# Optimization experiments

Measured on AMD Instinct MI355X. Metric: run time of the kernel, lower is better.

Reference implementation:

```python
import jax, jax.numpy as jnp
import numpy as np


def _attention(v, W, static_hidden, dec_hidden):
    # static_hidden: [B,N,H], dec_hidden: [B,1,H], v: [1,1,H], W: [1,H,2H]
    hidden = jnp.concatenate(
        [static_hidden, jnp.broadcast_to(dec_hidden, static_hidden.shape)], axis=2
    )  # [B,N,2H]
    e = jnp.tanh(jnp.einsum('bnk,hk->bnh', hidden, W[0]))  # W @ hidden^T, done row-wise
    scores = jnp.einsum('bnh,h->bn', e, v[0, 0])  # [B,N]
    return jax.nn.softmax(scores, axis=1)[:, None, :]  # [B,1,N]


def _gru_step(x, h, w_ih, w_hh, b_ih, b_hh):
    # x: [B,H] input, h: [B,H] prev hidden; PyTorch gate order: r | z | n
    gx = x @ w_ih.T + b_ih  # [B,3H]
    gh = h @ w_hh.T + b_hh  # [B,3H]
    H = h.shape[-1]
    r = jax.nn.sigmoid(gx[:, :H] + gh[:, :H])
    z = jax.nn.sigmoid(gx[:, H:2 * H] + gh[:, H:2 * H])
    n = jnp.tanh(gx[:, 2 * H:] + r * gh[:, 2 * H:])
    return (1.0 - z) * n + z * h


def _pointer_scores(v, W, static_hidden, context, state_embedding):
    # energy = cat(static, context, state_emb) -> [B,N,3H]
    energy = jnp.concatenate(
        [static_hidden,
         jnp.broadcast_to(context, static_hidden.shape),
         jnp.broadcast_to(state_embedding, static_hidden.shape)], axis=2)
    e = jnp.tanh(jnp.einsum('bnk,hk->bnh', energy, W[0]))  # [B,N,H]
    return jnp.einsum('bnh,h->bn', e, v[0, 0])  # [B,N]


def setup_inputs() -> dict:
    key = jax.random.key(0)
    B, N, H = 128, 512, 512
    ks = jax.random.split(key, 16)
    s = 0.05
    return {
        'static_hidden': jax.random.normal(ks[0], (B, N, H), jnp.float32),
        'state_embedding': jax.random.normal(ks[1], (B, 1, H), jnp.float32),
        'decoder_hidden': jax.random.normal(ks[2], (B, 1, H), jnp.float32),
        'target_hidden': jax.random.normal(ks[3], (B, 1, H), jnp.float32),
        'last_hh': jax.random.normal(ks[4], (1, B, H), jnp.float32),
        # Pointer params (note: target branch of the original reuses self.v/self.W)
        'ptr_v': jax.random.normal(ks[5], (1, 1, H), jnp.float32) * s,
        'ptr_W': jax.random.normal(ks[6], (1, H, 3 * H), jnp.float32) * s,
        # encoder attention params
        'enc_v': jax.random.normal(ks[7], (1, 1, H), jnp.float32) * s,
        'enc_W': jax.random.normal(ks[8], (1, H, 2 * H), jnp.float32) * s,
        # target attention params
        'tgt_v': jax.random.normal(ks[9], (1, 1, H), jnp.float32) * s,
        'tgt_W': jax.random.normal(ks[10], (1, H, 2 * H), jnp.float32) * s,
        # GRU (single layer) params
        'gru_w_ih': jax.random.normal(ks[11], (3 * H, H), jnp.float32) * s,
        'gru_w_hh': jax.random.normal(ks[12], (3 * H, H), jnp.float32) * s,
        'gru_b_ih': jax.random.normal(ks[13], (3 * H,), jnp.float32) * s,
        'gru_b_hh': jax.random.normal(ks[14], (3 * H,), jnp.float32) * s,
    }


def reference(static_hidden, state_embedding, decoder_hidden, target_hidden, last_hh,
              ptr_v, ptr_W, enc_v, enc_W, tgt_v, tgt_W,
              gru_w_ih, gru_w_hh, gru_b_ih, gru_b_hh):
    # GRU over seq len 1 (batch_first); dropout layers are identity (eval mode)
    h_new = _gru_step(decoder_hidden[:, 0, :], last_hh[0], gru_w_ih, gru_w_hh, gru_b_ih, gru_b_hh)
    rnn_out = h_new[:, None, :]          # [B,1,H]
    new_last_hh = h_new[None]            # [1,B,H]

    # encoder attention + context
    enc_attn = _attention(enc_v, enc_W, static_hidden, rnn_out)   # [B,1,N]
    context = jnp.matmul(enc_attn, static_hidden)                 # [B,1,H]
    probs = _pointer_scores(ptr_v, ptr_W, static_hidden, context, state_embedding)

    # target attention + context (original reuses self.v/self.W for scoring)
    tgt_attn = _attention(tgt_v, tgt_W, static_hidden, target_hidden)
    context_t = jnp.matmul(tgt_attn, static_hidden)
    probs_target = _pointer_scores(ptr_v, ptr_W, static_hidden, context_t, state_embedding)

    probs = 5.0 * probs + probs_target
    return (probs, new_last_hh)
```

## Files before the change

### kernel.cpp

```cpp
#include <hip/hip_runtime.h>
#include <math.h>

#define B 128
#define N 512
#define H 512

typedef __attribute__((ext_vector_type(8))) short short8;
typedef __attribute__((ext_vector_type(4))) float floatx4;

typedef const __attribute__((address_space(1))) unsigned int* gas_t;
typedef __attribute__((address_space(3))) unsigned int* las_t;

__device__ __forceinline__ void gl16(const void* g, void* l){
    __builtin_amdgcn_global_load_lds((gas_t)g, (las_t)l, 16, 0, 0);
}

__device__ __forceinline__ float sigmoidf_(float x){ return 1.0f/(1.0f+__expf(-x)); }

__device__ __forceinline__ float fast_tanh(float x){
    float t = __expf(-2.0f*fabsf(x));
    float r = __fdividef(1.0f - t, 1.0f + t);
    return copysignf(r, x);
}

__device__ __forceinline__ unsigned f2bf1(float f){
    unsigned u = __float_as_uint(f);
    u += 0x7FFFu + ((u>>16)&1u);
    return u>>16;
}
__device__ __forceinline__ unsigned pk2(float a, float b){
    return f2bf1(a) | (f2bf1(b)<<16);
}

__global__ __launch_bounds__(256) void k_cast_small(
    const float* __restrict__ encW, const float* __restrict__ tgtW,
    const float* __restrict__ ptrW, const float* __restrict__ wih,
    const float* __restrict__ whh,
    const float* __restrict__ dec, const float* __restrict__ lhh,
    const float* __restrict__ tgt, const float* __restrict__ sem,
    unsigned short* __restrict__ We_s, unsigned short* __restrict__ Wt_s,
    unsigned short* __restrict__ Wp_s, unsigned short* __restrict__ We_d,
    unsigned short* __restrict__ Wt_d, unsigned short* __restrict__ Wp_c,
    unsigned short* __restrict__ Wp_e, unsigned short* __restrict__ Wih_b,
    unsigned short* __restrict__ Whh_b,
    unsigned short* __restrict__ Xbf, unsigned short* __restrict__ Hbf,
    unsigned short* __restrict__ Tbf, unsigned short* __restrict__ Sbf)
{
    int r = blockIdx.x, t = threadIdx.x;
    if (r < 6656){
        const float* src; unsigned short* dst; int pitch, off, row;
        if (r < 512)      { src=encW; dst=We_s; pitch=2*H; off=0;   row=r; }
        else if (r<1024)  { src=tgtW; dst=Wt_s; pitch=2*H; off=0;   row=r-512; }
        else if (r<1536)  { src=ptrW; dst=Wp_s; pitch=3*H; off=0;   row=r-1024; }
        else if (r<2048)  { src=encW; dst=We_d; pitch=2*H; off=H;   row=r-1536; }
        else if (r<2560)  { src=tgtW; dst=Wt_d; pitch=2*H; off=H;   row=r-2048; }
        else if (r<3072)  { src=ptrW; dst=Wp_c; pitch=3*H; off=H;   row=r-2560; }
        else if (r<3584)  { src=ptrW; dst=Wp_e; pitch=3*H; off=2*H; row=r-3072; }
        else if (r<5120)  { src=wih;  dst=Wih_b;pitch=H;   off=0;   row=r-3584; }
        else              { src=whh;  dst=Whh_b;pitch=H;   off=0;   row=r-5120; }
        float2 v = *(const float2*)&src[(size_t)row*pitch + off + 2*t];
        *(unsigned*)&dst[(size_t)row*H + 2*t] = pk2(v.x, v.y);
    } else {
        int blk = r - 6656; int mat = blk >> 5;
        const float* src = mat==0?dec : mat==1?lhh : mat==2?tgt : sem;
        unsigned short* dst = mat==0?Xbf : mat==1?Hbf : mat==2?Tbf : Sbf;
        size_t i = ((size_t)(blk&31)*256 + t)*8;
        float4 lo = *(const float4*)&src[i];
        float4 hi = *(const float4*)&src[i+4];
        uint4 p;
        p.x = pk2(lo.x,lo.y); p.y = pk2(lo.z,lo.w);
        p.z = pk2(hi.x,hi.y); p.w = pk2(hi.z,hi.w);
        *(uint4*)&dst[i] = p;
    }
}

__device__ __forceinline__ void gemm128_tile(
    const unsigned short* __restrict__ Ab,
    const unsigned short* __restrict__ Bb,
    float* __restrict__ C, int ldc)
{
    __shared__ __align__(16) unsigned short As[128*64];
    __shared__ __align__(16) unsigned short Bs[128*64];
    int t = threadIdx.x;
    int lane = t & 63, wave = t >> 6;
    int wy = wave >> 1, wx = wave & 1;
    int li = lane & 15, quad = lane >> 4;

    floatx4 acc[4][4];
    #pragma unroll
    for (int i=0;i<4;++i)
      #pragma unroll
      for (int j=0;j<4;++j) acc[i][j] = (floatx4)(0.0f);

    for (int kt=0; kt<8; ++kt){
        int k0 = kt*64;
        #pragma unroll
        for (int c=0;c<4;++c){
            int s = c*256 + t;
            int row = s >> 3;
            int kb = (s & 7) ^ (row & 7);
            gl16(&Ab[(size_t)row*512 + k0 + kb*8], &As[(size_t)s*8]);
            gl16(&Bb[(size_t)row*512 + k0 + kb*8], &Bs[(size_t)s*8]);
        }
        __syncthreads();
        #pragma unroll
        for (int ks=0;ks<2;++ks){
            short8 af[4], bg[4];
            #pragma unroll
            for (int i=0;i<4;++i){
                int m = wy*64 + i*16 + li;
                int kb = (ks*4 + quad) ^ (m&7);
                af[i] = *(const short8*)&As[m*64 + kb*8];
            }
            #pragma unroll
            for (int j=0;j<4;++j){
                int h = wx*64 + j*16 + li;
                int kb = (ks*4 + quad) ^ (h&7);
                bg[j] = *(const short8*)&Bs[h*64 + kb*8];
            }
            #pragma unroll
            for (int i=0;i<4;++i)
              #pragma unroll
              for (int j=0;j<4;++j)
                acc[i][j] = __builtin_amdgcn_mfma_f32_16x16x32_bf16(af[i], bg[j], acc[i][j], 0,0,0);
        }
        __syncthreads();
    }
    #pragma unroll
    for (int i=0;i<4;++i)
      #pragma unroll
      for (int j=0;j<4;++j)
        #pragma unroll
        for (int rg=0;rg<4;++rg){
            int m = wy*64 + i*16 + quad*4 + rg;
            int n = wx*64 + j*16 + li;
            C[(size_t)m*ldc + n] = acc[i][j][rg];
        }
}

__device__ __forceinline__ void gemm128_tile_f32A(
    const float* __restrict__ Af,
    const unsigned short* __restrict__ Bb,
    float* __restrict__ C, int ldc)
{
    __shared__ __align__(16) unsigned short As[128*64];
    __shared__ __align__(16) unsigned short Bs[128*64];
    int t = threadIdx.x;
    int lane = t & 63, wave = t >> 6;
    int wy = wave >> 1, wx = wave & 1;
    int li = lane & 15, quad = lane >> 4;

    floatx4 acc[4][4];
    #pragma unroll
    for (int i=0;i<4;++i)
      #pragma unroll
      for (int j=0;j<4;++j) acc[i][j] = (floatx4)(0.0f);

    for (int kt=0; kt<8; ++kt){
        int k0 = kt*64;
        #pragma unroll
        for (int c=0;c<4;++c){
            int s = c*256 + t;
            int row = s >> 3;
            int kb = (s & 7) ^ (row & 7);
            gl16(&Bb[(size_t)row*512 + k0 + kb*8], &Bs[(size_t)s*8]);
            const float* src = Af + (size_t)row*512 + k0 + kb*8;
            float4 lo = *(const float4*)src;
            float4 hi = *(const float4*)(src+4);
            uint4 p;
            p.x = pk2(lo.x,lo.y); p.y = pk2(lo.z,lo.w);
            p.z = pk2(hi.x,hi.y); p.w = pk2(hi.z,hi.w);
            *(uint4*)&As[(size_t)s*8] = p;
        }
        __syncthreads();
        #pragma unroll
        for (int ks=0;ks<2;++ks){
            short8 af[4], bg[4];
            #pragma unroll
            for (int i=0;i<4;++i){
                int m = wy*64 + i*16 + li;
                int kb = (ks*4 + quad) ^ (m&7);
                af[i] = *(const short8*)&As[m*64 + kb*8];
            }
            #pragma unroll
            for (int j=0;j<4;++j){
                int h = wx*64 + j*16 + li;
                int kb = (ks*4 + quad) ^ (h&7);
                bg[j] = *(const short8*)&Bs[h*64 + kb*8];
            }
            #pragma unroll
            for (int i=0;i<4;++i)
              #pragma unroll
              for (int j=0;j<4;++j)
                acc[i][j] = __builtin_amdgcn_mfma_f32_16x16x32_bf16(af[i], bg[j], acc[i][j], 0,0,0);
        }
        __syncthreads();
    }
    #pragma unroll
    for (int i=0;i<4;++i)
      #pragma unroll
      for (int j=0;j<4;++j)
        #pragma unroll
        for (int rg=0;rg<4;++rg){
            int m = wy*64 + i*16 + quad*4 + rg;
            int n = wx*64 + j*16 + li;
            C[(size_t)m*ldc + n] = acc[i][j][rg];
        }
}

__global__ __launch_bounds__(256,2) void k_mega(
    const unsigned short* __restrict__ Xbf, const unsigned short* __restrict__ Hbf,
    const unsigned short* __restrict__ Wih_b, const unsigned short* __restrict__ Whh_b,
    float* __restrict__ gx, float* __restrict__ gh,
    const unsigned short* __restrict__ Tbf, const unsigned short* __restrict__ Sbf,
    const unsigned short* __restrict__ Wt_d, const unsigned short* __restrict__ Wp_e,
    float* __restrict__ d_tgt, float* __restrict__ d_se,
    const float* __restrict__ A, unsigned short* __restrict__ Abf)
{
    int blk = blockIdx.x;
    if (blk < 32){
        const unsigned short *Ab, *Bb; float* C; int ldc;
        if (blk < 24){
            int mat = blk / 12, nt = blk % 12;
            Ab = mat ? Hbf : Xbf;
            Bb = (mat ? Whh_b : Wih_b) + (size_t)nt*128*512;
            C = (mat ? gh : gx) + nt*128;
            ldc = 3*H;
        } else {
            int sub = blk - 24; int mat = sub >> 2, nt = sub & 3;
            Ab = mat==0 ? Tbf : Sbf;
            Bb = (mat==0 ? Wt_d : Wp_e) + (size_t)nt*128*512;
            C = (mat==0 ? d_tgt : d_se) + nt*128;
            ldc = H;
        }
        gemm128_tile(Ab, Bb, C, ldc);
    } else {
        int t = threadIdx.x;
        size_t i = ((size_t)(blk-32)*256 + t)*8;
        float4 lo = *(const float4*)&A[i];
        float4 hi = *(const float4*)&A[i+4];
        uint4 p;
        p.x = pk2(lo.x,lo.y); p.y = pk2(lo.z,lo.w);
        p.z = pk2(hi.x,hi.y); p.w = pk2(hi.z,hi.w);
        *(uint4*)&Abf[i] = p;
    }
}

__global__ __launch_bounds__(256) void k_gru_gate(const float* __restrict__ gx,
    const float* __restrict__ gh, const float* __restrict__ lhh,
    const float* __restrict__ bih, const float* __restrict__ bhh,
    float* __restrict__ out_hh, unsigned short* __restrict__ hnew_bf)
{
    int idx = blockIdx.x*256 + threadIdx.x;
    int b = idx >> 9, k = idx & 511;
    const float* gxb = gx + (size_t)b*(3*H);
    const float* ghb = gh + (size_t)b*(3*H);
    float r = sigmoidf_(gxb[k]     + bih[k]     + ghb[k]     + bhh[k]);
    float z = sigmoidf_(gxb[H+k]   + bih[H+k]   + ghb[H+k]   + bhh[H+k]);
    float n = tanhf(gxb[2*H+k] + bih[2*H+k] + r*(ghb[2*H+k] + bhh[2*H+k]));
    float h = (1.f-z)*n + z*lhh[idx];
    out_hh[idx] = h;
    hnew_bf[idx] = (unsigned short)f2bf1(h);
}

__global__ __launch_bounds__(256,2) void k_bias_enc(
    const unsigned short* __restrict__ HNbf, const unsigned short* __restrict__ We_d,
    float* __restrict__ d_enc)
{
    int nt = blockIdx.x;
    gemm128_tile(HNbf, We_d + (size_t)nt*128*512, d_enc + nt*128, H);
}

__global__ __launch_bounds__(256,2) void k_dptr_gemm(
    const float* __restrict__ ctx, const float* __restrict__ ctxt,
    const unsigned short* __restrict__ Wp_c,
    float* __restrict__ d_pe, float* __restrict__ d_pt)
{
    int blk = blockIdx.x;
    int mat = blk >> 2, nt = blk & 3;
    const float* Af = mat ? ctxt : ctx;
    const unsigned short* Bb = Wp_c + (size_t)nt*128*512;
    float* C = (mat ? d_pt : d_pe) + nt*128;
    gemm128_tile_f32A(Af, Bb, C, H);
}

template<bool BF16A>
__global__ __launch_bounds__(256,2) void k_scores_fused(
    const float* __restrict__ Af, const unsigned short* __restrict__ Abf,
    const unsigned short* __restrict__ We, const unsigned short* __restrict__ Wt,
    const float* __restrict__ d_enc, const float* __restrict__ d_tgt,
    const float* __restrict__ enc_v, const float* __restrict__ tgt_v,
    float* __restrict__ sc_e, float* __restrict__ sc_t)
{
    __shared__ __align__(16) unsigned short As[128*64];
    __shared__ __align__(16) unsigned short Be[128*64];
    __shared__ __align__(16) unsigned short Bt[128*64];
    __shared__ float red_e[2][128], red_t[2][128];
    int blk = blockIdx.x;
    int b = blk >> 2; int nt = blk & 3;
    int n0 = nt*128;
    int t = threadIdx.x;
    int lane = t & 63, wave = t >> 6;
    int wy = wave >> 1, wx = wave & 1;
    int li = lane & 15, quad = lane >> 4;

    float nse[4][4], nst[4][4];
    #pragma unroll
    for (int i=0;i<4;++i)
      #pragma unroll
      for (int rg=0;rg<4;++rg){ nse[i][rg]=0.f; nst[i][rg]=0.f; }

    for (int ht=0; ht<4; ++ht){
        int hb = ht*128;
        floatx4 acc_e[4][4], acc_t[4][4];
        #pragma unroll
        for (int i=0;i<4;++i)
          #pragma unroll
          for (int j=0;j<4;++j){ acc_e[i][j]=(floatx4)(0.0f); acc_t[i][j]=(floatx4)(0.0f); }

        for (int kt=0; kt<8; ++kt){
            int k0 = kt*64;
            #pragma unroll
            for (int c=0;c<4;++c){
                int s = c*256 + t;
                int row = s >> 3;
                int kb = (s & 7) ^ (row & 7);
                if constexpr (BF16A){
                    gl16(&Abf[(size_t)(b*N+n0+row)*H + k0 + kb*8], &As[(size_t)s*8]);
                } else {
                    const float* src = Af + (size_t)(b*N+n0+row)*H + k0 + kb*8;
                    float4 lo = *(const float4*)src;
                    float4 hi = *(const float4*)(src+4);
                    uint4 p;
                    p.x = pk2(lo.x,lo.y); p.y = pk2(lo.z,lo.w);
                    p.z = pk2(hi.x,hi.y); p.w = pk2(hi.z,hi.w);
                    *(uint4*)&As[(size_t)s*8] = p;
                }
                gl16(&We[(size_t)(hb+row)*H + k0 + kb*8], &Be[(size_t)s*8]);
                gl16(&Wt[(size_t)(hb+row)*H + k0 + kb*8], &Bt[(size_t)s*8]);
            }
            __syncthreads();
            #pragma unroll
            for (int ks=0;ks<2;++ks){
                short8 af[4], be[4], bt[4];
                #pragma unroll
                for (int i=0;i<4;++i){
                    int m = wy*64 + i*16 + li;
                    int kb = (ks*4 + quad) ^ (m&7);
                    af[i] = *(const short8*)&As[m*64 + kb*8];
                }
                #pragma unroll
                for (int j=0;j<4;++j){
                    int h = wx*64 + j*16 + li;
                    int kb = (ks*4 + quad) ^ (h&7);
                    be[j] = *(const short8*)&Be[h*64 + kb*8];
                    bt[j] = *(const short8*)&Bt[h*64 + kb*8];
                }
                #pragma unroll
                for (int i=0;i<4;++i)
                  #pragma unroll
                  for (int j=0;j<4;++j){
                    acc_e[i][j] = __builtin_amdgcn_mfma_f32_16x16x32_bf16(af[i], be[j], acc_e[i][j], 0,0,0);
                    acc_t[i][j] = __builtin_amdgcn_mfma_f32_16x16x32_bf16(af[i], bt[j], acc_t[i][j], 0,0,0);
                  }
            }
            __syncthreads();
        }
        #pragma unroll
        for (int j=0;j<4;++j){
            int hm = hb + wx*64 + j*16 + li;
            float dje = d_enc[b*H+hm], vje = enc_v[hm];
            float djt = d_tgt[b*H+hm], vjt = tgt_v[hm];
            #pragma unroll
            for (int i=0;i<4;++i)
              #pragma unroll
              for (int rg=0;rg<4;++rg){
                nse[i][rg] += vje * fast_tanh(acc_e[i][j][rg] + dje);
                nst[i][rg] += vjt * fast_tanh(acc_t[i][j][rg] + djt);
              }
        }
    }
    #pragma unroll
    for (int off=1; off<16; off<<=1)
      #pragma unroll
      for (int i=0;i<4;++i)
        #pragma unroll
        for (int rg=0;rg<4;++rg){
          nse[i][rg] += __shfl_xor(nse[i][rg], off);
          nst[i][rg] += __shfl_xor(nst[i][rg], off);
        }
    if (li==0){
        #pragma unroll
        for (int i=0;i<4;++i)
          #pragma unroll
          for (int rg=0;rg<4;++rg){
            red_e[wx][wy*64 + i*16 + quad*4 + rg] = nse[i][rg];
            red_t[wx][wy*64 + i*16 + quad*4 + rg] = nst[i][rg];
          }
    }
    __syncthreads();
    if (t < 128){
        sc_e[b*N + n0 + t] = red_e[0][t] + red_e[1][t];
    } else {
        int r2 = t - 128;
        sc_t[b*N + n0 + r2] = red_t[0][r2] + red_t[1][r2];
    }
}

template<bool BF16A>
__global__ __launch_bounds__(256) void k_smax_ctx(
    const float* __restrict__ Af, const unsigned short* __restrict__ Abf,
    const float* __restrict__ sc_e, const float* __restrict__ sc_t,
    float* __restrict__ ctx, float* __restrict__ ctxt)
{
    __shared__ float we[512], wt[512];
    __shared__ float buf[256];
    __shared__ float red[4][64][4];
    int b = blockIdx.x >> 2, q = blockIdx.x & 3;
    int t = threadIdx.x;

    {
        float x0 = sc_e[b*N+t], x1 = sc_e[b*N+t+256];
        float m = fmaxf(x0,x1);
        buf[t]=m; __syncthreads();
        for (int s2=128;s2>0;s2>>=1){ if(t<s2) buf[t]=fmaxf(buf[t],buf[t+s2]); __syncthreads(); }
        m = buf[0]; __syncthreads();
        float e0 = __expf(x0-m), e1 = __expf(x1-m);
        buf[t]=e0+e1; __syncthreads();
        for (int s2=128;s2>0;s2>>=1){ if(t<s2) buf[t]+=buf[t+s2]; __syncthreads(); }
        float inv = 1.0f/buf[0]; __syncthreads();
        we[t]=e0*inv; we[t+256]=e1*inv;
    }
    {
        float x0 = sc_t[b*N+t], x1 = sc_t[b*N+t+256];
        float m = fmaxf(x0,x1);
        buf[t]=m; __syncthreads();
        for (int s2=128;s2>0;s2>>=1){ if(t<s2) buf[t]=fmaxf(buf[t],buf[t+s2]); __syncthreads(); }
        m = buf[0]; __syncthreads();
        float e0 = __expf(x0-m), e1 = __expf(x1-m);
        buf[t]=e0+e1; __syncthreads();
        for (int s2=128;s2>0;s2>>=1){ if(t<s2) buf[t]+=buf[t+s2]; __syncthreads(); }
        float inv = 1.0f/buf[0]; __syncthreads();
        wt[t]=e0*inv; wt[t+256]=e1*inv;
    }
    __syncthreads();

    int p = t & 63, nq = t >> 6;
    int cp = q*64 + p;
    float ae0=0.f, ae1=0.f, at0=0.f, at1=0.f;
    if constexpr (BF16A){
        const unsigned* base = (const unsigned*)Abf + (size_t)(b*N + nq*128)*(H/2) + cp;
        for (int n=0;n<128;++n){
            unsigned u = base[(size_t)n*(H/2)];
            float lo = __uint_as_float(u<<16);
            float hi = __uint_as_float(u & 0xFFFF0000u);
            float e = we[nq*128+n], g = wt[nq*128+n];
            ae0 += e*lo; ae1 += e*hi; at0 += g*lo; at1 += g*hi;
        }
    } else {
        const float* base = Af + (size_t)(b*N + nq*128)*H + 2*cp;
        for (int n=0;n<128;++n){
            float2 v = *(const float2*)&base[(size_t)n*H];
            float e = we[nq*128+n], g = wt[nq*128+n];
            ae0 += e*v.x; ae1 += e*v.y; at0 += g*v.x; at1 += g*v.y;
        }
    }
    red[nq][p][0]=ae0; red[nq][p][1]=ae1; red[nq][p][2]=at0; red[nq][p][3]=at1;
    __syncthreads();
    if (t < 64){
        float s0=0.f,s1=0.f,s2=0.f,s3=0.f;
        #pragma unroll
        for (int k2=0;k2<4;++k2){
            s0+=red[k2][t][0]; s1+=red[k2][t][1]; s2+=red[k2][t][2]; s3+=red[k2][t][3];
        }
        int c2 = q*64 + t;
        ctx [(size_t)b*H + 2*c2]   = s0;
        ctx [(size_t)b*H + 2*c2+1] = s1;
        ctxt[(size_t)b*H + 2*c2]   = s2;
        ctxt[(size_t)b*H + 2*c2+1] = s3;
    }
}

template<bool BF16A>
__global__ __launch_bounds__(256,2) void k_probs_mfma(
    const float* __restrict__ Af, const unsigned short* __restrict__ Abf,
    const unsigned short* __restrict__ Wp,
    const float* __restrict__ d_pe, const float* __restrict__ d_pt,
    const float* __restrict__ d_se,
    const float* __restrict__ ptr_v, float* __restrict__ probs)
{
    __shared__ __align__(16) unsigned short As[128*64];
    __shared__ __align__(16) unsigned short Bs[128*64];
    __shared__ float red[2][128];
    int blk = blockIdx.x;
    int b = blk >> 2; int nt = blk & 3;
    int n0 = nt*128;

    int t = threadIdx.x;
    int lane = t & 63, wave = t >> 6;
    int wy = wave >> 1, wx = wave & 1;
    int li = lane & 15, quad = lane >> 4;

    float nsum[4][4];
    #pragma unroll
    for (int i=0;i<4;++i){ nsum[i][0]=0.f;nsum[i][1]=0.f;nsum[i][2]=0.f;nsum[i][3]=0.f; }

    for (int ht=0; ht<4; ++ht){
        int hb = ht*128;
        floatx4 acc[4][4];
        #pragma unroll
        for (int i=0;i<4;++i)
          #pragma unroll
          for (int j=0;j<4;++j) acc[i][j] = (floatx4)(0.0f);

        for (int kt=0; kt<8; ++kt){
            int k0 = kt*64;
            #pragma unroll
            for (int c=0;c<4;++c){
                int s = c*256 + t;
                int row = s >> 3;
                int kb = (s & 7) ^ (row & 7);
                if constexpr (BF16A){
                    gl16(&Abf[(size_t)(b*N+n0+row)*H + k0 + kb*8], &As[(size_t)s*8]);
                } else {
                    const float* src = Af + (size_t)(b*N+n0+row)*H + k0 + kb*8;
                    float4 lo = *(const float4*)src;
                    float4 hi = *(const float4*)(src+4);
                    uint4 p;
                    p.x = pk2(lo.x,lo.y); p.y = pk2(lo.z,lo.w);
                    p.z = pk2(hi.x,hi.y); p.w = pk2(hi.z,hi.w);
                    *(uint4*)&As[(size_t)s*8] = p;
                }
                gl16(&Wp[(size_t)(hb+row)*H + k0 + kb*8], &Bs[(size_t)s*8]);
            }
            __syncthreads();
            #pragma unroll
            for (int ks=0;ks<2;++ks){
                short8 af[4], bg[4];
                #pragma unroll
                for (int i=0;i<4;++i){
                    int m = wy*64 + i*16 + li;
                    int kb = (ks*4 + quad) ^ (m&7);
                    af[i] = *(const short8*)&As[m*64 + kb*8];
                }
                #pragma unroll
                for (int j=0;j<4;++j){
                    int h = wx*64 + j*16 + li;
                    int kb = (ks*4 + quad) ^ (h&7);
                    bg[j] = *(const short8*)&Bs[h*64 + kb*8];
                }
                #pragma unroll
                for (int i=0;i<4;++i)
                  #pragma unroll
                  for (int j=0;j<4;++j)
                    acc[i][j] = __builtin_amdgcn_mfma_f32_16x16x32_bf16(af[i], bg[j], acc[i][j], 0,0,0);
            }
            __syncthreads();
        }
        #pragma unroll
        for (int j=0;j<4;++j){
            int hm = hb + wx*64 + j*16 + li;
            float se = d_se[b*H + hm];
            float de = d_pe[b*H + hm] + se;
            float dt = d_pt[b*H + hm] + se;
            float vj = ptr_v[hm];
            #pragma unroll
            for (int i=0;i<4;++i)
              #pragma unroll
              for (int rg=0;rg<4;++rg){
                float s = acc[i][j][rg];
                nsum[i][rg] += vj * (5.0f*fast_tanh(s + de) + fast_tanh(s + dt));
              }
        }
    }
    #pragma unroll
    for (int off=1; off<16; off<<=1)
      #pragma unroll
      for (int i=0;i<4;++i)
        #pragma unroll
        for (int rg=0;rg<4;++rg)
          nsum[i][rg] += __shfl_xor(nsum[i][rg], off);
    if (li==0){
        #pragma unroll
        for (int i=0;i<4;++i)
          #pragma unroll
          for (int rg=0;rg<4;++rg)
            red[wx][wy*64 + i*16 + quad*4 + rg] = nsum[i][rg];
    }
    __syncthreads();
    if (t < 128)
        probs[b*N + n0 + t] = red[0][t] + red[1][t];
}

extern "C" void kernel_launch(void* const* d_in, const int* in_sizes, int n_in,
                              void* d_out, int out_size, void* d_ws, size_t ws_size,
                              hipStream_t stream)
{
    (void)in_sizes; (void)n_in; (void)out_size;
    const float* A    = (const float*)d_in[0];
    const float* sem  = (const float*)d_in[1];
    const float* dec  = (const float*)d_in[2];
    const float* tgt  = (const float*)d_in[3];
    const float* lhh  = (const float*)d_in[4];
    const float* ptrv = (const float*)d_in[5];
    const float* ptrW = (const float*)d_in[6];
    const float* encv = (const float*)d_in[7];
    const float* encW = (const float*)d_in[8];
    const float* tgtv = (const float*)d_in[9];
    const float* tgtW = (const float*)d_in[10];
    const float* wih  = (const float*)d_in[11];
    const float* whh  = (const float*)d_in[12];
    const float* bih  = (const float*)d_in[13];
    const float* bhh  = (const float*)d_in[14];

    float* probs_out = (float*)d_out;
    float* hh_out    = (float*)d_out + B*N;

    float* ws = (float*)d_ws;
    const size_t S = (size_t)B*H;
    float* d_enc = ws;
    float* d_tgt = ws + S;
    float* d_se  = ws + 2*S;
    float* sc_e  = ws + 3*S;
    float* sc_t  = ws + 4*S;
    float* ctx   = ws + 5*S;
    float* ctxt  = ws + 6*S;
    float* d_pe  = ws + 9*S;
    float* d_pt  = ws + 10*S;
    float* gx    = ws + 11*S;
    float* gh    = ws + 14*S;
    unsigned short* bfb  = (unsigned short*)(ws + 17*S);
    const size_t WH = (size_t)H*H;
    const size_t WG = (size_t)3*H*H;
    unsigned short* We_s  = bfb;
    unsigned short* Wt_s  = We_s + WH;
    unsigned short* Wp_s  = Wt_s + WH;
    unsigned short* We_d  = Wp_s + WH;
    unsigned short* Wt_d  = We_d + WH;
    unsigned short* Wp_c  = Wt_d + WH;
    unsigned short* Wp_e  = Wp_c + WH;
    unsigned short* Wih_b = Wp_e + WH;
    unsigned short* Whh_b = Wih_b + WG;
    unsigned short* Xbf   = Whh_b + WG;
    unsigned short* Hbf   = Xbf + S;
    unsigned short* Tbf   = Hbf + S;
    unsigned short* Sbf   = Tbf + S;
    unsigned short* HNbf  = Sbf + S;
    unsigned short* Abf   = HNbf + S;

    const size_t need_full = 17*S*sizeof(float)
        + (7*WH + 2*WG + 5*S + (size_t)B*N*H) * sizeof(unsigned short);
    const bool big = ws_size >= need_full;

    k_cast_small<<<6784, 256, 0, stream>>>(encW, tgtW, ptrW, wih, whh,
        dec, lhh, tgt, sem,
        We_s, Wt_s, Wp_s, We_d, Wt_d, Wp_c, Wp_e, Wih_b, Whh_b,
        Xbf, Hbf, Tbf, Sbf);

    int castA_blocks = big ? (int)(((size_t)B*N*H)/(256*8)) : 0;
    k_mega<<<32 + castA_blocks, 256, 0, stream>>>(Xbf, Hbf, Wih_b, Whh_b, gx, gh,
        Tbf, Sbf, Wt_d, Wp_e, d_tgt, d_se, A, Abf);

    k_gru_gate<<<256, 256, 0, stream>>>(gx, gh, lhh, bih, bhh, hh_out, HNbf);

    k_bias_enc<<<4, 256, 0, stream>>>(HNbf, We_d, d_enc);

    if (big)
        k_scores_fused<true ><<<512, 256, 0, stream>>>(A, Abf, We_s, Wt_s, d_enc, d_tgt, encv, tgtv, sc_e, sc_t);
    else
        k_scores_fused<false><<<512, 256, 0, stream>>>(A, Abf, We_s, Wt_s, d_enc, d_tgt, encv, tgtv, sc_e, sc_t);

    if (big)
        k_smax_ctx<true ><<<512, 256, 0, stream>>>(A, Abf, sc_e, sc_t, ctx, ctxt);
    else
        k_smax_ctx<false><<<512, 256, 0, stream>>>(A, Abf, sc_e, sc_t, ctx, ctxt);

    k_dptr_gemm<<<8, 256, 0, stream>>>(ctx, ctxt, Wp_c, d_pe, d_pt);

    if (big)
        k_probs_mfma<true ><<<512, 256, 0, stream>>>(A, Abf, Wp_s, d_pe, d_pt, d_se, ptrv, probs_out);
    else
        k_probs_mfma<false><<<512, 256, 0, stream>>>(A, Abf, Wp_s, d_pe, d_pt, d_se, ptrv, probs_out);
}
```

Baseline: 438.9 us.

## Double-buffer LDS in score/prob GEMMs and split-K the small GEMMs with atomics

The two large fused MFMA kernels now use double-buffered shared-memory tiles with a 32-wide K step, so global-to-LDS loads for the next step are issued while the current step computes, with one barrier per step. The small bias GEMMs (k_bias_enc, k_dptr_gemm) are split along K into four slices accumulated with atomicAdd, which launches more blocks, and their outputs are zeroed with memsets first. fast_tanh is simplified to a single exp plus divide. In exchange, atomic accumulation makes the results nondeterministic, the extra memset calls add launch overhead, and the new tanh form may lose precision near zero.

```diff
diff --git a/kernel.cpp b/kernel.cpp
--- a/kernel.cpp
+++ b/kernel.cpp
@@ -18,9 +18,8 @@
 __device__ __forceinline__ float sigmoidf_(float x){ return 1.0f/(1.0f+__expf(-x)); }
 
 __device__ __forceinline__ float fast_tanh(float x){
-    float t = __expf(-2.0f*fabsf(x));
-    float r = __fdividef(1.0f - t, 1.0f + t);
-    return copysignf(r, x);
+    float e = __expf(2.0f*x);
+    return 1.0f - __fdividef(2.0f, 1.0f + e);
 }
 
 __device__ __forceinline__ unsigned f2bf1(float f){
@@ -138,10 +137,10 @@
         }
 }
 
-__device__ __forceinline__ void gemm128_tile_f32A(
-    const float* __restrict__ Af,
+__device__ __forceinline__ void gemm128_kslice(
+    const unsigned short* __restrict__ Ab,
     const unsigned short* __restrict__ Bb,
-    float* __restrict__ C, int ldc)
+    float* __restrict__ C, int ldc, int ktbeg, int ktend)
 {
     __shared__ __align__(16) unsigned short As[128*64];
     __shared__ __align__(16) unsigned short Bs[128*64];
@@ -156,7 +155,71 @@
       #pragma unroll
       for (int j=0;j<4;++j) acc[i][j] = (floatx4)(0.0f);
 
-    for (int kt=0; kt<8; ++kt){
+    for (int kt=ktbeg; kt<ktend; ++kt){
+        int k0 = kt*64;
+        #pragma unroll
+        for (int c=0;c<4;++c){
+            int s = c*256 + t;
+            int row = s >> 3;
+            int kb = (s & 7) ^ (row & 7);
+            gl16(&Ab[(size_t)row*512 + k0 + kb*8], &As[(size_t)s*8]);
+            gl16(&Bb[(size_t)row*512 + k0 + kb*8], &Bs[(size_t)s*8]);
+        }
+        __syncthreads();
+        #pragma unroll
+        for (int ks=0;ks<2;++ks){
+            short8 af[4], bg[4];
+            #pragma unroll
+            for (int i=0;i<4;++i){
+                int m = wy*64 + i*16 + li;
+                int kb = (ks*4 + quad) ^ (m&7);
+                af[i] = *(const short8*)&As[m*64 + kb*8];
+            }
+            #pragma unroll
+            for (int j=0;j<4;++j){
+                int h = wx*64 + j*16 + li;
+                int kb = (ks*4 + quad) ^ (h&7);
+                bg[j] = *(const short8*)&Bs[h*64 + kb*8];
+            }
+            #pragma unroll
+            for (int i=0;i<4;++i)
+              #pragma unroll
+              for (int j=0;j<4;++j)
+                acc[i][j] = __builtin_amdgcn_mfma_f32_16x16x32_bf16(af[i], bg[j], acc[i][j], 0,0,0);
+        }
+        __syncthreads();
+    }
+    #pragma unroll
+    for (int i=0;i<4;++i)
+      #pragma unroll
+      for (int j=0;j<4;++j)
+        #pragma unroll
+        for (int rg=0;rg<4;++rg){
+            int m = wy*64 + i*16 + quad*4 + rg;
+            int n = wx*64 + j*16 + li;
+            atomicAdd(&C[(size_t)m*ldc + n], acc[i][j][rg]);
+        }
+}
+
+__device__ __forceinline__ void gemm128_kslice_f32A(
+    const float* __restrict__ Af,
+    const unsigned short* __restrict__ Bb,
+    float* __restrict__ C, int ldc, int ktbeg, int ktend)
+{
+    __shared__ __align__(16) unsigned short As[128*64];
+    __shared__ __align__(16) unsigned short Bs[128*64];
+    int t = threadIdx.x;
+    int lane = t & 63, wave = t >> 6;
+    int wy = wave >> 1, wx = wave & 1;
+    int li = lane & 15, quad = lane >> 4;
+
+    floatx4 acc[4][4];
+    #pragma unroll
+    for (int i=0;i<4;++i)
+      #pragma unroll
+      for (int j=0;j<4;++j) acc[i][j] = (floatx4)(0.0f);
+
+    for (int kt=ktbeg; kt<ktend; ++kt){
         int k0 = kt*64;
         #pragma unroll
         for (int c=0;c<4;++c){
@@ -204,7 +267,7 @@
         for (int rg=0;rg<4;++rg){
             int m = wy*64 + i*16 + quad*4 + rg;
             int n = wx*64 + j*16 + li;
-            C[(size_t)m*ldc + n] = acc[i][j][rg];
+            atomicAdd(&C[(size_t)m*ldc + n], acc[i][j][rg]);
         }
 }
 
@@ -267,8 +330,8 @@
     const unsigned short* __restrict__ HNbf, const unsigned short* __restrict__ We_d,
     float* __restrict__ d_enc)
 {
-    int nt = blockIdx.x;
-    gemm128_tile(HNbf, We_d + (size_t)nt*128*512, d_enc + nt*128, H);
+    int nt = blockIdx.x & 3, ks = blockIdx.x >> 2;
+    gemm128_kslice(HNbf, We_d + (size_t)nt*128*512, d_enc + nt*128, H, ks*2, ks*2+2);
 }
 
 __global__ __launch_bounds__(256,2) void k_dptr_gemm(
@@ -277,11 +340,12 @@
     float* __restrict__ d_pe, float* __restrict__ d_pt)
 {
     int blk = blockIdx.x;
-    int mat = blk >> 2, nt = blk & 3;
+    int mat = blk >> 4, sub = blk & 15;
+    int nt = sub & 3, ks = sub >> 2;
     const float* Af = mat ? ctxt : ctx;
     const unsigned short* Bb = Wp_c + (size_t)nt*128*512;
     float* C = (mat ? d_pt : d_pe) + nt*128;
-    gemm128_tile_f32A(Af, Bb, C, H);
+    gemm128_kslice_f32A(Af, Bb, C, H, ks*2, ks*2+2);
 }
 
 template<bool BF16A>
@@ -292,9 +356,9 @@
     const float* __restrict__ enc_v, const float* __restrict__ tgt_v,
     float* __restrict__ sc_e, float* __restrict__ sc_t)
 {
-    __shared__ __align__(16) unsigned short As[128*64];
-    __shared__ __align__(16) unsigned short Be[128*64];
-    __shared__ __align__(16) unsigned short Bt[128*64];
+    __shared__ __align__(16) unsigned short As[2][128*32];
+    __shared__ __align__(16) unsigned short Be[2][128*32];
+    __shared__ __align__(16) unsigned short Bt[2][128*32];
     __shared__ float red_e[2][128], red_t[2][128];
     int blk = blockIdx.x;
     int b = blk >> 2; int nt = blk & 3;
@@ -310,62 +374,66 @@
       #pragma unroll
       for (int rg=0;rg<4;++rg){ nse[i][rg]=0.f; nst[i][rg]=0.f; }
 
+    auto stage = [&](int pb, int ht, int kt){
+        int hb = ht*128, k0 = kt*32;
+        #pragma unroll
+        for (int c=0;c<2;++c){
+            int s = c*256 + t;
+            int row = s >> 2;
+            int kb = (s & 3) ^ ((row >> 2) & 3);
+            if constexpr (BF16A){
+                gl16(&Abf[(size_t)(b*N+n0+row)*H + k0 + kb*8], &As[pb][(size_t)s*8]);
+            } else {
+                const float* src = Af + (size_t)(b*N+n0+row)*H + k0 + kb*8;
+                float4 lo = *(const float4*)src;
+                float4 hi = *(const float4*)(src+4);
+                uint4 pq;
+                pq.x = pk2(lo.x,lo.y); pq.y = pk2(lo.z,lo.w);
+                pq.z = pk2(hi.x,hi.y); pq.w = pk2(hi.z,hi.w);
+                *(uint4*)&As[pb][(size_t)s*8] = pq;
+            }
+            gl16(&We[(size_t)(hb+row)*H + k0 + kb*8], &Be[pb][(size_t)s*8]);
+            gl16(&Wt[(size_t)(hb+row)*H + k0 + kb*8], &Bt[pb][(size_t)s*8]);
+        }
+    };
+
+    stage(0, 0, 0);
+    int p = 0;
     for (int ht=0; ht<4; ++ht){
-        int hb = ht*128;
         floatx4 acc_e[4][4], acc_t[4][4];
         #pragma unroll
         for (int i=0;i<4;++i)
           #pragma unroll
           for (int j=0;j<4;++j){ acc_e[i][j]=(floatx4)(0.0f); acc_t[i][j]=(floatx4)(0.0f); }
 
-        for (int kt=0; kt<8; ++kt){
-            int k0 = kt*64;
-            #pragma unroll
-            for (int c=0;c<4;++c){
-                int s = c*256 + t;
-                int row = s >> 3;
-                int kb = (s & 7) ^ (row & 7);
-                if constexpr (BF16A){
-                    gl16(&Abf[(size_t)(b*N+n0+row)*H + k0 + kb*8], &As[(size_t)s*8]);
-                } else {
-                    const float* src = Af + (size_t)(b*N+n0+row)*H + k0 + kb*8;
-                    float4 lo = *(const float4*)src;
-                    float4 hi = *(const float4*)(src+4);
-                    uint4 p;
-                    p.x = pk2(lo.x,lo.y); p.y = pk2(lo.z,lo.w);
-                    p.z = pk2(hi.x,hi.y); p.w = pk2(hi.z,hi.w);
-                    *(uint4*)&As[(size_t)s*8] = p;
-                }
-                gl16(&We[(size_t)(hb+row)*H + k0 + kb*8], &Be[(size_t)s*8]);
-                gl16(&Wt[(size_t)(hb+row)*H + k0 + kb*8], &Bt[(size_t)s*8]);
-            }
+        for (int kt=0; kt<16; ++kt){
             __syncthreads();
-            #pragma unroll
-            for (int ks=0;ks<2;++ks){
-                short8 af[4], be[4], bt[4];
-                #pragma unroll
-                for (int i=0;i<4;++i){
-                    int m = wy*64 + i*16 + li;
-                    int kb = (ks*4 + quad) ^ (m&7);
-                    af[i] = *(const short8*)&As[m*64 + kb*8];
-                }
-                #pragma unroll
-                for (int j=0;j<4;++j){
-                    int h = wx*64 + j*16 + li;
-                    int kb = (ks*4 + quad) ^ (h&7);
-                    be[j] = *(const short8*)&Be[h*64 + kb*8];
-                    bt[j] = *(const short8*)&Bt[h*64 + kb*8];
-                }
-                #pragma unroll
-                for (int i=0;i<4;++i)
-                  #pragma unroll
-                  for (int j=0;j<4;++j){
-                    acc_e[i][j] = __builtin_amdgcn_mfma_f32_16x16x32_bf16(af[i], be[j], acc_e[i][j], 0,0,0);
-                    acc_t[i][j] = __builtin_amdgcn_mfma_f32_16x16x32_bf16(af[i], bt[j], acc_t[i][j], 0,0,0);
-                  }
-            }
-            __syncthreads();
-        }
+            if (kt < 15)      stage(p^1, ht, kt+1);
+            else if (ht < 3)  stage(p^1, ht+1, 0);
+            short8 af[4], bev[4], btv[4];
+            #pragma unroll
+            for (int i=0;i<4;++i){
+                int m = wy*64 + i*16 + li;
+                int kb = quad ^ ((m>>2)&3);
+                af[i] = *(const short8*)&As[p][m*32 + kb*8];
+            }
+            #pragma unroll
+            for (int j=0;j<4;++j){
+                int h2 = wx*64 + j*16 + li;
+                int kb = quad ^ ((h2>>2)&3);
+                bev[j] = *(const short8*)&Be[p][h2*32 + kb*8];
+                btv[j] = *(const short8*)&Bt[p][h2*32 + kb*8];
+            }
+            #pragma unroll
+            for (int i=0;i<4;++i)
+              #pragma unroll
+              for (int j=0;j<4;++j){
+                acc_e[i][j] = __builtin_amdgcn_mfma_f32_16x16x32_bf16(af[i], bev[j], acc_e[i][j], 0,0,0);
+                acc_t[i][j] = __builtin_amdgcn_mfma_f32_16x16x32_bf16(af[i], btv[j], acc_t[i][j], 0,0,0);
+              }
+            p ^= 1;
+        }
+        int hb = ht*128;
         #pragma unroll
         for (int j=0;j<4;++j){
             int hm = hb + wx*64 + j*16 + li;
@@ -489,8 +557,8 @@
     const float* __restrict__ d_se,
     const float* __restrict__ ptr_v, float* __restrict__ probs)
 {
-    __shared__ __align__(16) unsigned short As[128*64];
-    __shared__ __align__(16) unsigned short Bs[128*64];
+    __shared__ __align__(16) unsigned short As[2][128*32];
+    __shared__ __align__(16) unsigned short Bs[2][128*32];
     __shared__ float red[2][128];
     int blk = blockIdx.x;
     int b = blk >> 2; int nt = blk & 3;
@@ -505,58 +573,62 @@
     #pragma unroll
     for (int i=0;i<4;++i){ nsum[i][0]=0.f;nsum[i][1]=0.f;nsum[i][2]=0.f;nsum[i][3]=0.f; }
 
+    auto stage = [&](int pb, int ht, int kt){
+        int hb = ht*128, k0 = kt*32;
+        #pragma unroll
+        for (int c=0;c<2;++c){
+            int s = c*256 + t;
+            int row = s >> 2;
+            int kb = (s & 3) ^ ((row >> 2) & 3);
+            if constexpr (BF16A){
+                gl16(&Abf[(size_t)(b*N+n0+row)*H + k0 + kb*8], &As[pb][(size_t)s*8]);
+            } else {
+                const float* src = Af + (size_t)(b*N+n0+row)*H + k0 + kb*8;
+                float4 lo = *(const float4*)src;
+                float4 hi = *(const float4*)(src+4);
+                uint4 pq;
+                pq.x = pk2(lo.x,lo.y); pq.y = pk2(lo.z,lo.w);
+                pq.z = pk2(hi.x,hi.y); pq.w = pk2(hi.z,hi.w);
+                *(uint4*)&As[pb][(size_t)s*8] = pq;
+            }
+            gl16(&Wp[(size_t)(hb+row)*H + k0 + kb*8], &Bs[pb][(size_t)s*8]);
+        }
+    };
+
+    stage(0, 0, 0);
+    int p = 0;
     for (int ht=0; ht<4; ++ht){
-        int hb = ht*128;
         floatx4 acc[4][4];
         #pragma unroll
         for (int i=0;i<4;++i)
           #pragma unroll
           for (int j=0;j<4;++j) acc[i][j] = (floatx4)(0.0f);
 
-        for (int kt=0; kt<8; ++kt){
-            int k0 = kt*64;
-            #pragma unroll
-            for (int c=0;c<4;++c){
-                int s = c*256 + t;
-                int row = s >> 3;
-                int kb = (s & 7) ^ (row & 7);
-                if constexpr (BF16A){
-                    gl16(&Abf[(size_t)(b*N+n0+row)*H + k0 + kb*8], &As[(size_t)s*8]);
-                } else {
-                    const float* src = Af + (size_t)(b*N+n0+row)*H + k0 + kb*8;
-                    float4 lo = *(const float4*)src;
-                    float4 hi = *(const float4*)(src+4);
-                    uint4 p;
-                    p.x = pk2(lo.x,lo.y); p.y = pk2(lo.z,lo.w);
-                    p.z = pk2(hi.x,hi.y); p.w = pk2(hi.z,hi.w);
-                    *(uint4*)&As[(size_t)s*8] = p;
-                }
-                gl16(&Wp[(size_t)(hb+row)*H + k0 + kb*8], &Bs[(size_t)s*8]);
-            }
+        for (int kt=0; kt<16; ++kt){
             __syncthreads();
-            #pragma unroll
-            for (int ks=0;ks<2;++ks){
-                short8 af[4], bg[4];
-                #pragma unroll
-                for (int i=0;i<4;++i){
-                    int m = wy*64 + i*16 + li;
-                    int kb = (ks*4 + quad) ^ (m&7);
-                    af[i] = *(const short8*)&As[m*64 + kb*8];
-                }
-                #pragma unroll
-                for (int j=0;j<4;++j){
-                    int h = wx*64 + j*16 + li;
-                    int kb = (ks*4 + quad) ^ (h&7);
-                    bg[j] = *(const short8*)&Bs[h*64 + kb*8];
-                }
-                #pragma unroll
-                for (int i=0;i<4;++i)
-                  #pragma unroll
-                  for (int j=0;j<4;++j)
-                    acc[i][j] = __builtin_amdgcn_mfma_f32_16x16x32_bf16(af[i], bg[j], acc[i][j], 0,0,0);
-            }
-            __syncthreads();
-        }
+            if (kt < 15)      stage(p^1, ht, kt+1);
+            else if (ht < 3)  stage(p^1, ht+1, 0);
+            short8 af[4], bg[4];
+            #pragma unroll
+            for (int i=0;i<4;++i){
+                int m = wy*64 + i*16 + li;
+                int kb = quad ^ ((m>>2)&3);
+                af[i] = *(const short8*)&As[p][m*32 + kb*8];
+            }
+            #pragma unroll
+            for (int j=0;j<4;++j){
+                int h2 = wx*64 + j*16 + li;
+                int kb = quad ^ ((h2>>2)&3);
+                bg[j] = *(const short8*)&Bs[p][h2*32 + kb*8];
+            }
+            #pragma unroll
+            for (int i=0;i<4;++i)
+              #pragma unroll
+              for (int j=0;j<4;++j)
+                acc[i][j] = __builtin_amdgcn_mfma_f32_16x16x32_bf16(af[i], bg[j], acc[i][j], 0,0,0);
+            p ^= 1;
+        }
+        int hb = ht*128;
         #pragma unroll
         for (int j=0;j<4;++j){
             int hm = hb + wx*64 + j*16 + li;
@@ -652,6 +724,9 @@
         + (7*WH + 2*WG + 5*S + (size_t)B*N*H) * sizeof(unsigned short);
     const bool big = ws_size >= need_full;
 
+    hipMemsetAsync(d_enc, 0, S*sizeof(float), stream);
+    hipMemsetAsync(d_pe, 0, 2*S*sizeof(float), stream);
+
     k_cast_small<<<6784, 256, 0, stream>>>(encW, tgtW, ptrW, wih, whh,
         dec, lhh, tgt, sem,
         We_s, Wt_s, Wp_s, We_d, Wt_d, Wp_c, Wp_e, Wih_b, Whh_b,
@@ -663,7 +738,7 @@
 
     k_gru_gate<<<256, 256, 0, stream>>>(gx, gh, lhh, bih, bhh, hh_out, HNbf);
 
-    k_bias_enc<<<4, 256, 0, stream>>>(HNbf, We_d, d_enc);
+    k_bias_enc<<<16, 256, 0, stream>>>(HNbf, We_d, d_enc);
 
     if (big)
         k_scores_fused<true ><<<512, 256, 0, stream>>>(A, Abf, We_s, Wt_s, d_enc, d_tgt, encv, tgtv, sc_e, sc_t);
@@ -675,7 +750,7 @@
     else
         k_smax_ctx<false><<<512, 256, 0, stream>>>(A, Abf, sc_e, sc_t, ctx, ctxt);
 
-    k_dptr_gemm<<<8, 256, 0, stream>>>(ctx, ctxt, Wp_c, d_pe, d_pt);
+    k_dptr_gemm<<<32, 256, 0, stream>>>(ctx, ctxt, Wp_c, d_pe, d_pt);
 
     if (big)
         k_probs_mfma<true ><<<512, 256, 0, stream>>>(A, Abf, Wp_s, d_pe, d_pt, d_se, ptrv, probs_out);
```

Result: no change. 438.8 us (-0.0%).
